# Performance work log

Measured on AMD Instinct MI355X. Metric: run time of the kernel, lower is better.

## Reference

```python
import jax, jax.numpy as jnp
import numpy as np

B, FIN, NK, FOUT = 4096, 64, 512, 256

def setup_inputs() -> dict:
    key = jax.random.key(0)
    k1, k2, k3, k4 = jax.random.split(key, 4)
    input = jax.random.normal(k1, (B, FIN), dtype=jnp.float32)
    # xavier_uniform on [FOUT, NK]
    bound = float(np.sqrt(6.0 / (FOUT + NK)))
    weights = jax.random.uniform(k2, (FOUT, NK), minval=-bound, maxval=bound, dtype=jnp.float32)
    kernels_centers = jax.random.uniform(k3, (NK, FIN), minval=-1.0, maxval=1.0, dtype=jnp.float32)
    log_shapes = 0.1 * jax.random.normal(k4, (NK,), dtype=jnp.float32)
    return {"input": input, "weights": weights, "kernels_centers": kernels_centers, "log_shapes": log_shapes}

def reference(input, weights, kernels_centers, log_shapes):
    # diff: [B, NK, FIN]
    diff = input[:, None, :] - kernels_centers[None, :, :]
    # Euclidean norm over feature dim -> r: [B, NK]
    r = jnp.sqrt(jnp.sum(diff * diff, axis=-1))
    eps_r = jnp.exp(log_shapes)[None, :] * r
    # Gaussian radial function phi(x) = exp(-x^2)
    rbfs = jnp.exp(-(eps_r * eps_r))
    # normalization
    rbfs = rbfs / (1e-9 + jnp.sum(rbfs, axis=-1, keepdims=True))
    # out[b,o] = sum_k weights[o,k] * rbfs[b,k]
    out = jnp.einsum("ok,bk->bo", weights, rbfs)
    return out
```

## Files before the change

kernel.cpp:

```cpp
#include <hip/hip_runtime.h>
#include <math.h>

#define FIN   64
#define NK    512
#define FOUT  256
#define BB    16
#define NTHR  1024
#define RSTRH 520

typedef __attribute__((ext_vector_type(8))) short short8;
typedef __attribute__((ext_vector_type(4))) float f32x4;
typedef unsigned short ushort_t;

#define MFMA(a, b, c) __builtin_amdgcn_mfma_f32_16x16x32_bf16((a), (b), (c), 0, 0, 0)

#define XHI   0
#define XMID  262144
#define XLO   524288
#define CHI   786432
#define CMID  819200
#define CLO   851968
#define WHI   884736
#define WLO   1015808
#define USH_END 1146880
#define CSQ_F 0
#define E2_F  512
#define XSQ_F 1024

__device__ __forceinline__ ushort_t top16(float f) {
    return (ushort_t)(__builtin_bit_cast(unsigned, f) >> 16);
}
__device__ __forceinline__ float trunc_bf(float f) {
    return __builtin_bit_cast(float, __builtin_bit_cast(unsigned, f) & 0xFFFF0000u);
}

__global__ __launch_bounds__(256) void rbf_prep_kernel(
    const float* __restrict__ x, const float* __restrict__ w,
    const float* __restrict__ cent, const float* __restrict__ ls,
    ushort_t* __restrict__ us, float* __restrict__ fs)
{
    const int gid = blockIdx.x * 256 + threadIdx.x;
    const int nth = gridDim.x * 256;

    for (int i = gid; i < 4096 * FIN; i += nth) {
        const float v = x[i];
        const float m1 = v - trunc_bf(v);
        const float l1 = m1 - trunc_bf(m1);
        us[XHI + i]  = top16(v);
        us[XMID + i] = top16(m1);
        us[XLO + i]  = top16(l1);
    }
    for (int i = gid; i < NK * FIN; i += nth) {
        const float v = cent[i];
        const float m1 = v - trunc_bf(v);
        const float l1 = m1 - trunc_bf(m1);
        us[CHI + i]  = top16(v);
        us[CMID + i] = top16(m1);
        us[CLO + i]  = top16(l1);
    }
    for (int i = gid; i < FOUT * NK; i += nth) {
        const float v = w[i];
        const float l1 = v - trunc_bf(v);
        us[WHI + i] = top16(v);
        us[WLO + i] = top16(l1);
    }
    for (int r = gid; r < 4096; r += nth) {
        const float4* xp = (const float4*)(x + (size_t)r * FIN);
        float s = 0.f;
        #pragma unroll
        for (int j = 0; j < 16; ++j) {
            const float4 c = xp[j];
            s = fmaf(c.x, c.x, s); s = fmaf(c.y, c.y, s);
            s = fmaf(c.z, c.z, s); s = fmaf(c.w, c.w, s);
        }
        fs[XSQ_F + r] = s;
    }
    for (int k = gid; k < NK; k += nth) {
        const float4* cp = (const float4*)(cent + (size_t)k * FIN);
        float s = 0.f;
        #pragma unroll
        for (int j = 0; j < 16; ++j) {
            const float4 c = cp[j];
            s = fmaf(c.x, c.x, s); s = fmaf(c.y, c.y, s);
            s = fmaf(c.z, c.z, s); s = fmaf(c.w, c.w, s);
        }
        fs[CSQ_F + k] = s;
        fs[E2_F + k]  = __expf(2.f * ls[k]);
    }
}

__global__ __launch_bounds__(NTHR, 1) void rbf_main_kernel(
    const ushort_t* __restrict__ us, const float* __restrict__ fs,
    float* __restrict__ out)
{
    __shared__ __align__(16) ushort_t RsHi[BB][RSTRH];
    __shared__ __align__(16) ushort_t RsLo[BB][RSTRH];
    __shared__ float rowpart[16][BB];
    __shared__ float invs[BB];

    const int tid   = threadIdx.x;
    const int lane  = tid & 63;
    const int wv    = tid >> 6;
    const int arow  = lane & 15;
    const int dg    = lane >> 4;
    const int d0    = dg * 8;
    const int rbase = dg * 4;
    const int b0    = blockIdx.x * BB;

    const int xoff = (b0 + arow) * FIN;
    const short8 ax1_0 = *(const short8*)&us[XHI  + xoff + d0];
    const short8 ax1_1 = *(const short8*)&us[XHI  + xoff + 32 + d0];
    const short8 ax2_0 = *(const short8*)&us[XMID + xoff + d0];
    const short8 ax2_1 = *(const short8*)&us[XMID + xoff + 32 + d0];
    const short8 ax3_0 = *(const short8*)&us[XLO  + xoff + d0];
    const short8 ax3_1 = *(const short8*)&us[XLO  + xoff + 32 + d0];

    const float xq0 = fs[XSQ_F + b0 + rbase + 0];
    const float xq1 = fs[XSQ_F + b0 + rbase + 1];
    const float xq2 = fs[XSQ_F + b0 + rbase + 2];
    const float xq3 = fs[XSQ_F + b0 + rbase + 3];

    float ps0 = 0.f, ps1 = 0.f, ps2 = 0.f, ps3 = 0.f;
    #pragma unroll 1
    for (int i = 0; i < 2; ++i) {
        const int col  = 32 * wv + 16 * i + arow;
        const int coff = col * FIN;
        const short8 b1_0 = *(const short8*)&us[CHI  + coff + d0];
        const short8 b1_1 = *(const short8*)&us[CHI  + coff + 32 + d0];
        const short8 b2_0 = *(const short8*)&us[CMID + coff + d0];
        const short8 b2_1 = *(const short8*)&us[CMID + coff + 32 + d0];
        const short8 b3_0 = *(const short8*)&us[CLO  + coff + d0];
        const short8 b3_1 = *(const short8*)&us[CLO  + coff + 32 + d0];
        const float cq = fs[CSQ_F + col];
        const float e2 = fs[E2_F + col];

        f32x4 acc = {0.f, 0.f, 0.f, 0.f};
        acc = MFMA(ax1_0, b1_0, acc);
        acc = MFMA(ax1_0, b2_0, acc);
        acc = MFMA(ax2_0, b1_0, acc);
        acc = MFMA(ax2_0, b2_0, acc);
        acc = MFMA(ax1_0, b3_0, acc);
        acc = MFMA(ax3_0, b1_0, acc);
        acc = MFMA(ax1_1, b1_1, acc);
        acc = MFMA(ax1_1, b2_1, acc);
        acc = MFMA(ax2_1, b1_1, acc);
        acc = MFMA(ax2_1, b2_1, acc);
        acc = MFMA(ax1_1, b3_1, acc);
        acc = MFMA(ax3_1, b1_1, acc);

        {
            const float ssq = fmaf(-2.f, acc[0], xq0 + cq);
            const float rb = __expf(-(e2 * ssq));
            ps0 += rb;
            RsHi[rbase + 0][col] = top16(rb);
            RsLo[rbase + 0][col] = top16(rb - trunc_bf(rb));
        }
        {
            const float ssq = fmaf(-2.f, acc[1], xq1 + cq);
            const float rb = __expf(-(e2 * ssq));
            ps1 += rb;
            RsHi[rbase + 1][col] = top16(rb);
            RsLo[rbase + 1][col] = top16(rb - trunc_bf(rb));
        }
        {
            const float ssq = fmaf(-2.f, acc[2], xq2 + cq);
            const float rb = __expf(-(e2 * ssq));
            ps2 += rb;
            RsHi[rbase + 2][col] = top16(rb);
            RsLo[rbase + 2][col] = top16(rb - trunc_bf(rb));
        }
        {
            const float ssq = fmaf(-2.f, acc[3], xq3 + cq);
            const float rb = __expf(-(e2 * ssq));
            ps3 += rb;
            RsHi[rbase + 3][col] = top16(rb);
            RsLo[rbase + 3][col] = top16(rb - trunc_bf(rb));
        }
    }
    ps0 += __shfl_xor(ps0, 1); ps0 += __shfl_xor(ps0, 2); ps0 += __shfl_xor(ps0, 4); ps0 += __shfl_xor(ps0, 8);
    ps1 += __shfl_xor(ps1, 1); ps1 += __shfl_xor(ps1, 2); ps1 += __shfl_xor(ps1, 4); ps1 += __shfl_xor(ps1, 8);
    ps2 += __shfl_xor(ps2, 1); ps2 += __shfl_xor(ps2, 2); ps2 += __shfl_xor(ps2, 4); ps2 += __shfl_xor(ps2, 8);
    ps3 += __shfl_xor(ps3, 1); ps3 += __shfl_xor(ps3, 2); ps3 += __shfl_xor(ps3, 4); ps3 += __shfl_xor(ps3, 8);
    if (arow == 0) {
        rowpart[wv][rbase + 0] = ps0;
        rowpart[wv][rbase + 1] = ps1;
        rowpart[wv][rbase + 2] = ps2;
        rowpart[wv][rbase + 3] = ps3;
    }
    __syncthreads();
    if (tid < BB) {
        float s = 0.f;
        #pragma unroll
        for (int q = 0; q < 16; ++q) s += rowpart[q][tid];
        invs[tid] = 1.f / (1e-9f + s);
    }
    __syncthreads();

    const int c0 = 16 * wv;
    const int w0off = (c0 + arow) * NK;

    f32x4 o0 = {0.f, 0.f, 0.f, 0.f};
    #pragma unroll 2
    for (int ks = 0; ks < NK / 32; ++ks) {
        const int kb = ks * 32 + d0;
        const short8 ahi = *(const short8*)&RsHi[arow][kb];
        const short8 alo = *(const short8*)&RsLo[arow][kb];
        const short8 w0h = *(const short8*)&us[WHI + w0off + kb];
        const short8 w0l = *(const short8*)&us[WLO + w0off + kb];
        o0 = MFMA(ahi, w0h, o0);
        o0 = MFMA(ahi, w0l, o0);
        o0 = MFMA(alo, w0h, o0);
    }

    #pragma unroll
    for (int j = 0; j < 4; ++j) {
        const int row = rbase + j;
        out[(size_t)(b0 + row) * FOUT + c0 + arow] = o0[j] * invs[row];
    }
}

extern "C" void kernel_launch(void* const* d_in, const int* in_sizes, int n_in,
                              void* d_out, int out_size, void* d_ws, size_t ws_size,
                              hipStream_t stream) {
    const float* x    = (const float*)d_in[0];
    const float* w    = (const float*)d_in[1];
    const float* cent = (const float*)d_in[2];
    const float* ls   = (const float*)d_in[3];
    float* out        = (float*)d_out;

    ushort_t* us = (ushort_t*)d_ws;
    float*    fs = (float*)(us + USH_END);

    rbf_prep_kernel<<<dim3(1024), dim3(256), 0, stream>>>(x, w, cent, ls, us, fs);
    rbf_main_kernel<<<dim3(4096 / BB), dim3(NTHR), 0, stream>>>(us, fs, out);
}
```

Before: 90.27 us.

## Process 32 batch rows per block and vectorize bf16 split prep

The main kernel now handles 32 batch rows per block in two 16-row groups. Each centre fragment and each weight fragment loaded from global memory is therefore reused across twice as many rows, and the grid halves to 128 blocks. The prep kernel packs eight elements per thread with float4 loads and 16-byte stores instead of scalar stores, and its grid shrinks to 256 blocks. The trade-off is fewer blocks than CUs on the main kernel and more registers per thread.

```diff
diff --git a/kernel.cpp b/kernel.cpp
--- a/kernel.cpp
+++ b/kernel.cpp
@@ -4,11 +4,12 @@
 #define FIN   64
 #define NK    512
 #define FOUT  256
-#define BB    16
+#define BB    32
 #define NTHR  1024
 #define RSTRH 520
 
 typedef __attribute__((ext_vector_type(8))) short short8;
+typedef __attribute__((ext_vector_type(8))) unsigned short ushort8;
 typedef __attribute__((ext_vector_type(4))) float f32x4;
 typedef unsigned short ushort_t;
 
@@ -34,6 +35,8 @@
     return __builtin_bit_cast(float, __builtin_bit_cast(unsigned, f) & 0xFFFF0000u);
 }
 
+union U8 { ushort_t a[8]; ushort8 v; };
+
 __global__ __launch_bounds__(256) void rbf_prep_kernel(
     const float* __restrict__ x, const float* __restrict__ w,
     const float* __restrict__ cent, const float* __restrict__ ls,
@@ -42,27 +45,58 @@
     const int gid = blockIdx.x * 256 + threadIdx.x;
     const int nth = gridDim.x * 256;
 
-    for (int i = gid; i < 4096 * FIN; i += nth) {
-        const float v = x[i];
-        const float m1 = v - trunc_bf(v);
-        const float l1 = m1 - trunc_bf(m1);
-        us[XHI + i]  = top16(v);
-        us[XMID + i] = top16(m1);
-        us[XLO + i]  = top16(l1);
-    }
-    for (int i = gid; i < NK * FIN; i += nth) {
-        const float v = cent[i];
-        const float m1 = v - trunc_bf(v);
-        const float l1 = m1 - trunc_bf(m1);
-        us[CHI + i]  = top16(v);
-        us[CMID + i] = top16(m1);
-        us[CLO + i]  = top16(l1);
-    }
-    for (int i = gid; i < FOUT * NK; i += nth) {
-        const float v = w[i];
-        const float l1 = v - trunc_bf(v);
-        us[WHI + i] = top16(v);
-        us[WLO + i] = top16(l1);
+    for (int t = gid; t < 4096 * FIN / 8; t += nth) {
+        const int i = t * 8;
+        const float4 a = *(const float4*)(x + i);
+        const float4 b = *(const float4*)(x + i + 4);
+        const float f[8] = {a.x, a.y, a.z, a.w, b.x, b.y, b.z, b.w};
+        U8 H, M, L;
+        #pragma unroll
+        for (int j = 0; j < 8; ++j) {
+            const float v  = f[j];
+            const float m1 = v - trunc_bf(v);
+            const float l1 = m1 - trunc_bf(m1);
+            H.a[j] = top16(v);
+            M.a[j] = top16(m1);
+            L.a[j] = top16(l1);
+        }
+        *(ushort8*)&us[XHI + i]  = H.v;
+        *(ushort8*)&us[XMID + i] = M.v;
+        *(ushort8*)&us[XLO + i]  = L.v;
+    }
+    for (int t = gid; t < NK * FIN / 8; t += nth) {
+        const int i = t * 8;
+        const float4 a = *(const float4*)(cent + i);
+        const float4 b = *(const float4*)(cent + i + 4);
+        const float f[8] = {a.x, a.y, a.z, a.w, b.x, b.y, b.z, b.w};
+        U8 H, M, L;
+        #pragma unroll
+        for (int j = 0; j < 8; ++j) {
+            const float v  = f[j];
+            const float m1 = v - trunc_bf(v);
+            const float l1 = m1 - trunc_bf(m1);
+            H.a[j] = top16(v);
+            M.a[j] = top16(m1);
+            L.a[j] = top16(l1);
+        }
+        *(ushort8*)&us[CHI + i]  = H.v;
+        *(ushort8*)&us[CMID + i] = M.v;
+        *(ushort8*)&us[CLO + i]  = L.v;
+    }
+    for (int t = gid; t < FOUT * NK / 8; t += nth) {
+        const int i = t * 8;
+        const float4 a = *(const float4*)(w + i);
+        const float4 b = *(const float4*)(w + i + 4);
+        const float f[8] = {a.x, a.y, a.z, a.w, b.x, b.y, b.z, b.w};
+        U8 H, L;
+        #pragma unroll
+        for (int j = 0; j < 8; ++j) {
+            const float v = f[j];
+            H.a[j] = top16(v);
+            L.a[j] = top16(v - trunc_bf(v));
+        }
+        *(ushort8*)&us[WHI + i] = H.v;
+        *(ushort8*)&us[WLO + i] = L.v;
     }
     for (int r = gid; r < 4096; r += nth) {
         const float4* xp = (const float4*)(x + (size_t)r * FIN);
@@ -107,23 +141,20 @@
     const int rbase = dg * 4;
     const int b0    = blockIdx.x * BB;
 
-    const int xoff = (b0 + arow) * FIN;
-    const short8 ax1_0 = *(const short8*)&us[XHI  + xoff + d0];
-    const short8 ax1_1 = *(const short8*)&us[XHI  + xoff + 32 + d0];
-    const short8 ax2_0 = *(const short8*)&us[XMID + xoff + d0];
-    const short8 ax2_1 = *(const short8*)&us[XMID + xoff + 32 + d0];
-    const short8 ax3_0 = *(const short8*)&us[XLO  + xoff + d0];
-    const short8 ax3_1 = *(const short8*)&us[XLO  + xoff + 32 + d0];
-
-    const float xq0 = fs[XSQ_F + b0 + rbase + 0];
-    const float xq1 = fs[XSQ_F + b0 + rbase + 1];
-    const float xq2 = fs[XSQ_F + b0 + rbase + 2];
-    const float xq3 = fs[XSQ_F + b0 + rbase + 3];
-
-    float ps0 = 0.f, ps1 = 0.f, ps2 = 0.f, ps3 = 0.f;
-    #pragma unroll 1
-    for (int i = 0; i < 2; ++i) {
-        const int col  = 32 * wv + 16 * i + arow;
+    float xq[8];
+    #pragma unroll
+    for (int rg = 0; rg < 2; ++rg)
+        #pragma unroll
+        for (int j = 0; j < 4; ++j)
+            xq[rg * 4 + j] = fs[XSQ_F + b0 + rg * 16 + rbase + j];
+
+    float ps[8];
+    #pragma unroll
+    for (int q = 0; q < 8; ++q) ps[q] = 0.f;
+
+    #pragma unroll
+    for (int ct = 0; ct < 2; ++ct) {
+        const int col  = 32 * wv + 16 * ct + arow;
         const int coff = col * FIN;
         const short8 b1_0 = *(const short8*)&us[CHI  + coff + d0];
         const short8 b1_1 = *(const short8*)&us[CHI  + coff + 32 + d0];
@@ -134,58 +165,54 @@
         const float cq = fs[CSQ_F + col];
         const float e2 = fs[E2_F + col];
 
-        f32x4 acc = {0.f, 0.f, 0.f, 0.f};
-        acc = MFMA(ax1_0, b1_0, acc);
-        acc = MFMA(ax1_0, b2_0, acc);
-        acc = MFMA(ax2_0, b1_0, acc);
-        acc = MFMA(ax2_0, b2_0, acc);
-        acc = MFMA(ax1_0, b3_0, acc);
-        acc = MFMA(ax3_0, b1_0, acc);
-        acc = MFMA(ax1_1, b1_1, acc);
-        acc = MFMA(ax1_1, b2_1, acc);
-        acc = MFMA(ax2_1, b1_1, acc);
-        acc = MFMA(ax2_1, b2_1, acc);
-        acc = MFMA(ax1_1, b3_1, acc);
-        acc = MFMA(ax3_1, b1_1, acc);
-
-        {
-            const float ssq = fmaf(-2.f, acc[0], xq0 + cq);
-            const float rb = __expf(-(e2 * ssq));
-            ps0 += rb;
-            RsHi[rbase + 0][col] = top16(rb);
-            RsLo[rbase + 0][col] = top16(rb - trunc_bf(rb));
-        }
-        {
-            const float ssq = fmaf(-2.f, acc[1], xq1 + cq);
-            const float rb = __expf(-(e2 * ssq));
-            ps1 += rb;
-            RsHi[rbase + 1][col] = top16(rb);
-            RsLo[rbase + 1][col] = top16(rb - trunc_bf(rb));
-        }
-        {
-            const float ssq = fmaf(-2.f, acc[2], xq2 + cq);
-            const float rb = __expf(-(e2 * ssq));
-            ps2 += rb;
-            RsHi[rbase + 2][col] = top16(rb);
-            RsLo[rbase + 2][col] = top16(rb - trunc_bf(rb));
-        }
-        {
-            const float ssq = fmaf(-2.f, acc[3], xq3 + cq);
-            const float rb = __expf(-(e2 * ssq));
-            ps3 += rb;
-            RsHi[rbase + 3][col] = top16(rb);
-            RsLo[rbase + 3][col] = top16(rb - trunc_bf(rb));
-        }
-    }
-    ps0 += __shfl_xor(ps0, 1); ps0 += __shfl_xor(ps0, 2); ps0 += __shfl_xor(ps0, 4); ps0 += __shfl_xor(ps0, 8);
-    ps1 += __shfl_xor(ps1, 1); ps1 += __shfl_xor(ps1, 2); ps1 += __shfl_xor(ps1, 4); ps1 += __shfl_xor(ps1, 8);
-    ps2 += __shfl_xor(ps2, 1); ps2 += __shfl_xor(ps2, 2); ps2 += __shfl_xor(ps2, 4); ps2 += __shfl_xor(ps2, 8);
-    ps3 += __shfl_xor(ps3, 1); ps3 += __shfl_xor(ps3, 2); ps3 += __shfl_xor(ps3, 4); ps3 += __shfl_xor(ps3, 8);
+        #pragma unroll
+        for (int rg = 0; rg < 2; ++rg) {
+            const int xoff = (b0 + rg * 16 + arow) * FIN;
+            const short8 a1_0 = *(const short8*)&us[XHI  + xoff + d0];
+            const short8 a1_1 = *(const short8*)&us[XHI  + xoff + 32 + d0];
+            const short8 a2_0 = *(const short8*)&us[XMID + xoff + d0];
+            const short8 a2_1 = *(const short8*)&us[XMID + xoff + 32 + d0];
+            const short8 a3_0 = *(const short8*)&us[XLO  + xoff + d0];
+            const short8 a3_1 = *(const short8*)&us[XLO  + xoff + 32 + d0];
+
+            f32x4 acc = {0.f, 0.f, 0.f, 0.f};
+            acc = MFMA(a1_0, b1_0, acc);
+            acc = MFMA(a1_0, b2_0, acc);
+            acc = MFMA(a2_0, b1_0, acc);
+            acc = MFMA(a2_0, b2_0, acc);
+            acc = MFMA(a1_0, b3_0, acc);
+            acc = MFMA(a3_0, b1_0, acc);
+            acc = MFMA(a1_1, b1_1, acc);
+            acc = MFMA(a1_1, b2_1, acc);
+            acc = MFMA(a2_1, b1_1, acc);
+            acc = MFMA(a2_1, b2_1, acc);
+            acc = MFMA(a1_1, b3_1, acc);
+            acc = MFMA(a3_1, b1_1, acc);
+
+            #pragma unroll
+            for (int j = 0; j < 4; ++j) {
+                const int rl = rg * 16 + rbase + j;
+                const float ssq = fmaf(-2.f, acc[j], xq[rg * 4 + j] + cq);
+                const float rb  = __expf(-(e2 * ssq));
+                ps[rg * 4 + j] += rb;
+                RsHi[rl][col] = top16(rb);
+                RsLo[rl][col] = top16(rb - trunc_bf(rb));
+            }
+        }
+    }
+    #pragma unroll
+    for (int q = 0; q < 8; ++q) {
+        ps[q] += __shfl_xor(ps[q], 1);
+        ps[q] += __shfl_xor(ps[q], 2);
+        ps[q] += __shfl_xor(ps[q], 4);
+        ps[q] += __shfl_xor(ps[q], 8);
+    }
     if (arow == 0) {
-        rowpart[wv][rbase + 0] = ps0;
-        rowpart[wv][rbase + 1] = ps1;
-        rowpart[wv][rbase + 2] = ps2;
-        rowpart[wv][rbase + 3] = ps3;
+        #pragma unroll
+        for (int rg = 0; rg < 2; ++rg)
+            #pragma unroll
+            for (int j = 0; j < 4; ++j)
+                rowpart[wv][rg * 16 + rbase + j] = ps[rg * 4 + j];
     }
     __syncthreads();
     if (tid < BB) {
@@ -196,26 +223,34 @@
     }
     __syncthreads();
 
-    const int c0 = 16 * wv;
-    const int w0off = (c0 + arow) * NK;
+    const int c0   = 16 * wv;
+    const int woff = (c0 + arow) * NK;
 
     f32x4 o0 = {0.f, 0.f, 0.f, 0.f};
-    #pragma unroll 2
-    for (int ks = 0; ks < NK / 32; ++ks) {
-        const int kb = ks * 32 + d0;
-        const short8 ahi = *(const short8*)&RsHi[arow][kb];
-        const short8 alo = *(const short8*)&RsLo[arow][kb];
-        const short8 w0h = *(const short8*)&us[WHI + w0off + kb];
-        const short8 w0l = *(const short8*)&us[WLO + w0off + kb];
-        o0 = MFMA(ahi, w0h, o0);
-        o0 = MFMA(ahi, w0l, o0);
-        o0 = MFMA(alo, w0h, o0);
+    f32x4 o1 = {0.f, 0.f, 0.f, 0.f};
+    #pragma unroll 4
+    for (int kp = 0; kp < NK / 32; ++kp) {
+        const int kb = kp * 32 + d0;
+        const short8 wh   = *(const short8*)&us[WHI + woff + kb];
+        const short8 wl   = *(const short8*)&us[WLO + woff + kb];
+        const short8 ahi0 = *(const short8*)&RsHi[arow][kb];
+        const short8 alo0 = *(const short8*)&RsLo[arow][kb];
+        const short8 ahi1 = *(const short8*)&RsHi[16 + arow][kb];
+        const short8 alo1 = *(const short8*)&RsLo[16 + arow][kb];
+        o0 = MFMA(ahi0, wh, o0);  o1 = MFMA(ahi1, wh, o1);
+        o0 = MFMA(ahi0, wl, o0);  o1 = MFMA(ahi1, wl, o1);
+        o0 = MFMA(alo0, wh, o0);  o1 = MFMA(alo1, wh, o1);
     }
 
     #pragma unroll
     for (int j = 0; j < 4; ++j) {
-        const int row = rbase + j;
-        out[(size_t)(b0 + row) * FOUT + c0 + arow] = o0[j] * invs[row];
+        const int r0 = rbase + j;
+        out[(size_t)(b0 + r0) * FOUT + c0 + arow] = o0[j] * invs[r0];
+    }
+    #pragma unroll
+    for (int j = 0; j < 4; ++j) {
+        const int r1 = 16 + rbase + j;
+        out[(size_t)(b0 + r1) * FOUT + c0 + arow] = o1[j] * invs[r1];
     }
 }
 
@@ -231,6 +266,6 @@
     ushort_t* us = (ushort_t*)d_ws;
     float*    fs = (float*)(us + USH_END);
 
-    rbf_prep_kernel<<<dim3(1024), dim3(256), 0, stream>>>(x, w, cent, ls, us, fs);
+    rbf_prep_kernel<<<dim3(256), dim3(256), 0, stream>>>(x, w, cent, ls, us, fs);
     rbf_main_kernel<<<dim3(4096 / BB), dim3(NTHR), 0, stream>>>(us, fs, out);
 }
```

Result: slower. 98.25 us (+8.8%).
